# Kernel optimization log

Hardware: AMD Instinct MI355X
Metric: run time of the kernel (lower is better)

The kernel has to match this reference:

```python
import jax, jax.numpy as jnp
import numpy as np

EPS = 1e-08
ROUTING_ITERS = 3

def squash(s, axis=-1):
    norm = jnp.linalg.norm(s, axis=axis, keepdims=True)
    return norm / (1.0 + norm ** 2 + EPS) * s

def setup_inputs() -> dict:
    key = jax.random.key(0)
    k1, k2, k3 = jax.random.split(key, 3)
    B, R, C, O, I = 512, 640, 10, 16, 8
    x = jax.random.normal(k1, (B, R, I), dtype=jnp.float32)
    W = jax.random.normal(k2, (R, C, O, I), dtype=jnp.float32) * 0.01
    bias = jax.random.uniform(k3, (1, 1, C, O), dtype=jnp.float32) * 0.01
    return {"x": x, "W": W, "bias": bias}

def reference(x, W, bias):
    # u_hat[b,r,c,o] = sum_i W[r,c,o,i] * x[b,r,i]
    u_hat = jnp.einsum('rcoi,bri->brco', W, x)  # [B,R,C,O]
    u_hat_d = jax.lax.stop_gradient(u_hat)
    B, R, C, _ = u_hat.shape
    b_ij = jnp.zeros((B, R, C, 1), dtype=u_hat.dtype)
    v_j = None
    for itr in range(ROUTING_ITERS):
        c_ij = jax.nn.softmax(b_ij, axis=2)               # softmax over capsules
        s_j = jnp.sum(c_ij * u_hat_d, axis=1, keepdims=True) + bias  # [B,1,C,O]
        v_j = squash(s_j, axis=-1)
        if itr < ROUTING_ITERS - 1:
            a_ij = jnp.sum(u_hat * v_j, axis=-1, keepdims=True)  # agreement, non-detached
            b_ij = b_ij + a_ij
    return jnp.squeeze(v_j, axis=1)  # [B,C,O]
```

## Files before the change

kernel.cpp:

```cpp
#include <hip/hip_runtime.h>
#include <math.h>

#define BB 512
#define RR 640
#define CC 10
#define OO 16
#define CO 160
#define II 8
#define S_FLOATS (BB*CO)

#define NRG 40
#define RPB 16
#define WCH (RPB*CO)
#define LSTR 165
#define VSTR 164
#define VOFF 10304
#define SMEM_FLOATS (VOFF + 16*VSTR)

#define NRG_FB 8
#define RPB_FB (RR/NRG_FB)
#define ZCH (RR*CO)

using f16x8 = __attribute__((ext_vector_type(8))) _Float16;
using f32x4 = __attribute__((ext_vector_type(4))) float;



__device__ __forceinline__ float exp_small(float a) {
    float f = __builtin_fmaf(a, 0.16666667f, 0.5f);
    f = __builtin_fmaf(a, f, 1.0f);
    return __builtin_fmaf(a, f, 1.0f);
}

__device__ __forceinline__ float rowsum16(float v) {
    int t;
    t = __builtin_amdgcn_update_dpp(0, __float_as_int(v), 0x128, 0xF, 0xF, true);
    v += __int_as_float(t);
    t = __builtin_amdgcn_update_dpp(0, __float_as_int(v), 0x124, 0xF, 0xF, true);
    v += __int_as_float(t);
    t = __builtin_amdgcn_update_dpp(0, __float_as_int(v), 0x122, 0xF, 0xF, true);
    v += __int_as_float(t);
    t = __builtin_amdgcn_update_dpp(0, __float_as_int(v), 0x121, 0xF, 0xF, true);
    v += __int_as_float(t);
    return v;
}


__global__ __launch_bounds__(256) void prep(const float* __restrict__ W,
                                            const float* __restrict__ x,
                                            _Float16* __restrict__ wf,
                                            _Float16* __restrict__ xf) {
    const int t = blockIdx.x * 256 + threadIdx.x;
    if (t < RR * CO * II) wf[t] = (_Float16)W[t];
    if (t < 16) wf[RR * CO * II + t] = (_Float16)0.f;
    const int i = t & 7;
    const int b = (t >> 3) & 511;
    const int r = t >> 12;
    xf[t] = (_Float16)x[((size_t)b * RR + r) * II + i];
}


template <bool UNIFORM>
__global__ __launch_bounds__(256) void caps_pass_l(const _Float16* __restrict__ wf,
                                                   const _Float16* __restrict__ xf,
                                                   const float* __restrict__ vacc,
                                                   float* __restrict__ part) {
    __shared__ float smem[SMEM_FLOATS];
    const int tid  = threadIdx.x;
    const int lane = tid & 63;
    const int wv   = tid >> 6;
    const int n    = lane & 15;
    const int q    = lane >> 4;
    const bool q0  = (q == 0);
    const int b0   = blockIdx.x * 16;
    const int rg   = blockIdx.y;
    const int r0   = rg * RPB;

    {
        const int4* wg = reinterpret_cast<const int4*>(wf) + (size_t)r0 * CO;
        int4* ws4 = reinterpret_cast<int4*>(smem);
#pragma unroll
        for (int k = 0; k < WCH / 256; ++k)
            ws4[k * 256 + tid] = wg[k * 256 + tid];
        if (tid == 0) { int4 z; z.x = z.y = z.z = z.w = 0; ws4[WCH] = z; }
        if (!UNIFORM) {
            const float4* vg = reinterpret_cast<const float4*>(vacc);
            for (int k = tid; k < 640; k += 256) {
                const int bl = k / 40, ch = k - bl * 40;
                const float4 v = vg[(size_t)(b0 + bl) * 40 + ch];
                *reinterpret_cast<float4*>(smem + VOFF + bl * VSTR + ch * 4) = v;
            }
        }
    }
    __syncthreads();

    const f16x8* xq  = reinterpret_cast<const f16x8*>(xf);
    const int4*  ws4 = reinterpret_cast<const int4*>(smem);

    f32x4 sacc[CC];
#pragma unroll
    for (int c = 0; c < CC; ++c) sacc[c] = (f32x4){0.f, 0.f, 0.f, 0.f};

    if (UNIFORM) {
        const int rl = 4 * wv + q;
        const f16x8 bfr = xq[(size_t)(r0 + rl) * BB + b0 + n];
#pragma unroll
        for (int c = 0; c < CC; ++c) {
            const int4 a = ws4[rl * CO + c * 16 + n];
            sacc[c] = __builtin_amdgcn_mfma_f32_16x16x32_f16(
                __builtin_bit_cast(f16x8, a), bfr, sacc[c], 0, 0, 0);
        }
    } else {
        const int rl0 = wv * 4;
        f16x8 xb[4];
#pragma unroll
        for (int j = 0; j < 4; ++j)
            xb[j] = xq[(size_t)(r0 + rl0 + j) * BB + b0 + n];
        const float* vb = smem + VOFF + n * VSTR + 4 * q;

#pragma unroll
        for (int j = 0; j < 4; ++j) {
            const int rl = rl0 + j;
            f32x4 acc[CC];
#pragma unroll
            for (int c = 0; c < CC; ++c) {
                const int4 a = ws4[q0 ? (rl * CO + c * 16 + n) : WCH];
                acc[c] = __builtin_amdgcn_mfma_f32_16x16x32_f16(
                    __builtin_bit_cast(f16x8, a), xb[j],
                    (f32x4){0.f, 0.f, 0.f, 0.f}, 0, 0, 0);
            }
            float e[CC];
#pragma unroll
            for (int c = 0; c < CC; ++c) {
                const f32x4 vv = *reinterpret_cast<const f32x4*>(vb + c * 16);
                float t = acc[c][0] * vv[0] + acc[c][1] * vv[1]
                        + acc[c][2] * vv[2] + acc[c][3] * vv[3];
                t += __shfl_xor(t, 16);
                t += __shfl_xor(t, 32);
                e[c] = exp_small(t);
            }
            const float se = (((e[0] + e[1]) + (e[2] + e[3]))
                            + ((e[4] + e[5]) + (e[6] + e[7]))) + (e[8] + e[9]);
            const float inv = __fdividef(1.0f, se);
#pragma unroll
            for (int c = 0; c < CC; ++c) {
                const float w = e[c] * inv;
#pragma unroll
                for (int k = 0; k < 4; ++k)
                    sacc[c][k] = __builtin_fmaf(w, acc[c][k], sacc[c][k]);
            }
        }
    }

    __syncthreads();
    float* red = smem;
    const int cb = 4 * q;
    if (wv < 2) {
        float* dst = red + ((wv * 16 + n) * LSTR + cb);
#pragma unroll
        for (int c = 0; c < CC; ++c)
#pragma unroll
            for (int k = 0; k < 4; ++k) dst[c * 16 + k] = sacc[c][k];
    }
    __syncthreads();
    if (wv >= 2) {
        float* dst = red + (((wv - 2) * 16 + n) * LSTR + cb);
#pragma unroll
        for (int c = 0; c < CC; ++c)
#pragma unroll
            for (int k = 0; k < 4; ++k) dst[c * 16 + k] += sacc[c][k];
    }
    __syncthreads();
    if (wv == 0) {
        const float f = UNIFORM ? 0.1f : 1.0f;
        float* pb = part + (size_t)rg * S_FLOATS + (size_t)(b0 + n) * CO + cb;
        const float* ra = red + (n * LSTR + cb);
        const float* rb = red + ((16 + n) * LSTR + cb);
#pragma unroll
        for (int c = 0; c < CC; ++c) {
            f32x4 v;
#pragma unroll
            for (int k = 0; k < 4; ++k)
                v[k] = (ra[c * 16 + k] + rb[c * 16 + k]) * f;
            *reinterpret_cast<f32x4*>(pb + c * 16) = v;
        }
    }
}

__global__ __launch_bounds__(256) void caps_squash(const float* __restrict__ part,
                                                   int nsl,
                                                   const float* __restrict__ bias,
                                                   float* __restrict__ vacc,
                                                   float* __restrict__ out,
                                                   int mode) {
    const int idx = blockIdx.x * 256 + threadIdx.x;
    const int co  = idx % CO;
    float a0 = 0.f, a1 = 0.f, a2 = 0.f, a3 = 0.f;
    int s = 0;
    for (; s + 4 <= nsl; s += 4) {
        a0 += part[(size_t)s * S_FLOATS + idx];
        a1 += part[(size_t)(s + 1) * S_FLOATS + idx];
        a2 += part[(size_t)(s + 2) * S_FLOATS + idx];
        a3 += part[(size_t)(s + 3) * S_FLOATS + idx];
    }
    for (; s < nsl; ++s) a0 += part[(size_t)s * S_FLOATS + idx];
    const float val = ((a0 + a1) + (a2 + a3)) + bias[co];
    const float sq = rowsum16(val * val);
    const float norm  = sqrtf(sq);
    const float scale = norm / (1.0f + sq + 1e-8f);
    const float v = scale * val;
    if (mode == 0)      vacc[idx] = v;
    else if (mode == 1) vacc[idx] += v;
    else                out[idx] = v;
}

template <bool UNIFORM, int RPB_>
__global__ __launch_bounds__(256, 2) void caps_pass_g(const _Float16* __restrict__ wf,
                                                      const _Float16* __restrict__ xf,
                                                      const float* __restrict__ vacc,
                                                      float* __restrict__ part) {
    __shared__ float red[2 * 16 * LSTR];
    const int tid  = threadIdx.x;
    const int lane = tid & 63;
    const int wv   = tid >> 6;
    const int n    = lane & 15;
    const int q    = lane >> 4;
    const bool q0  = (q == 0);
    const int b0   = blockIdx.x * 16;
    const int rg   = blockIdx.y;
    const int r0   = rg * RPB_;

    const f16x8* xq = reinterpret_cast<const f16x8*>(xf);
    const int4*  wq = reinterpret_cast<const int4*>(wf);

    f32x4 sacc[CC];
#pragma unroll
    for (int c = 0; c < CC; ++c) sacc[c] = (f32x4){0.f, 0.f, 0.f, 0.f};

    if (UNIFORM) {
#pragma unroll 2
        for (int rr = 4 * wv; rr + 4 <= RPB_; rr += 16) {
            const int r = r0 + rr + q;
            const f16x8 bfr = xq[(size_t)r * BB + b0 + n];
#pragma unroll
            for (int c = 0; c < CC; ++c) {
                const int4 a = wq[r * CO + c * 16 + n];
                sacc[c] = __builtin_amdgcn_mfma_f32_16x16x32_f16(
                    __builtin_bit_cast(f16x8, a), bfr, sacc[c], 0, 0, 0);
            }
        }
    } else {
        f32x4 vv[CC];
        const f32x4* vp = reinterpret_cast<const f32x4*>(vacc + (size_t)(b0 + n) * CO);
#pragma unroll
        for (int c = 0; c < CC; ++c) vv[c] = vp[c * 4 + q];
#pragma unroll 2
        for (int rr = wv; rr < RPB_; rr += 4) {
            const int r = r0 + rr;
            const f16x8 bcur = xq[(size_t)r * BB + b0 + n];
            f32x4 acc[CC];
#pragma unroll
            for (int c = 0; c < CC; ++c) {
                const int4 a = wq[q0 ? (r * CO + c * 16 + n) : ZCH];
                acc[c] = __builtin_amdgcn_mfma_f32_16x16x32_f16(
                    __builtin_bit_cast(f16x8, a), bcur,
                    (f32x4){0.f, 0.f, 0.f, 0.f}, 0, 0, 0);
            }
            float e[CC];
#pragma unroll
            for (int c = 0; c < CC; ++c) {
                float t = acc[c][0] * vv[c][0] + acc[c][1] * vv[c][1]
                        + acc[c][2] * vv[c][2] + acc[c][3] * vv[c][3];
                t += __shfl_xor(t, 16);
                t += __shfl_xor(t, 32);
                e[c] = exp_small(t);
            }
            const float se = (((e[0] + e[1]) + (e[2] + e[3]))
                            + ((e[4] + e[5]) + (e[6] + e[7]))) + (e[8] + e[9]);
            const float inv = __fdividef(1.0f, se);
#pragma unroll
            for (int c = 0; c < CC; ++c) {
                const float w = e[c] * inv;
#pragma unroll
                for (int k = 0; k < 4; ++k)
                    sacc[c][k] = __builtin_fmaf(w, acc[c][k], sacc[c][k]);
            }
        }
    }

    const int cb = 4 * q;
    if (wv < 2) {
        float* dst = red + ((wv * 16 + n) * LSTR + cb);
#pragma unroll
        for (int c = 0; c < CC; ++c)
#pragma unroll
            for (int k = 0; k < 4; ++k) dst[c * 16 + k] = sacc[c][k];
    }
    __syncthreads();
    if (wv >= 2) {
        float* dst = red + (((wv - 2) * 16 + n) * LSTR + cb);
#pragma unroll
        for (int c = 0; c < CC; ++c)
#pragma unroll
            for (int k = 0; k < 4; ++k) dst[c * 16 + k] += sacc[c][k];
    }
    __syncthreads();
    if (wv == 0) {
        const float f = UNIFORM ? 0.1f : 1.0f;
        float* pb = part + (size_t)rg * S_FLOATS + (size_t)(b0 + n) * CO + cb;
        const float* ra = red + (n * LSTR + cb);
        const float* rb = red + ((16 + n) * LSTR + cb);
#pragma unroll
        for (int c = 0; c < CC; ++c) {
            f32x4 v;
#pragma unroll
            for (int k = 0; k < 4; ++k)
                v[k] = (ra[c * 16 + k] + rb[c * 16 + k]) * f;
            *reinterpret_cast<f32x4*>(pb + c * 16) = v;
        }
    }
}


extern "C" void kernel_launch(void* const* d_in, const int* in_sizes, int n_in,
                              void* d_out, int out_size, void* d_ws, size_t ws_size,
                              hipStream_t stream) {
    const float* x    = (const float*)d_in[0];
    const float* W    = (const float*)d_in[1];
    const float* bias = (const float*)d_in[2];
    float* out  = (float*)d_out;

    const int sqg = S_FLOATS / 256;

    float*    part = (float*)d_ws;
    float*    vacc = part + (size_t)NRG * S_FLOATS;
    _Float16* wf   = (_Float16*)(vacc + S_FLOATS);
    _Float16* xf   = wf + (size_t)RR * CO * II + 16;

    const size_t NEEDED = ((size_t)NRG + 1) * S_FLOATS * 4
                        + ((size_t)RR * CO * II + 16) * 2
                        + (size_t)BB * RR * II * 2;

    if (ws_size >= NEEDED) {
        prep<<<BB * RR * II / 256, 256, 0, stream>>>(W, x, wf, xf);
        const dim3 pg(32, NRG);
        caps_pass_l<true ><<<pg, 256, 0, stream>>>(wf, xf, nullptr, part);
        caps_squash<<<sqg, 256, 0, stream>>>(part, NRG, bias, vacc, out, 0);
        caps_pass_l<false><<<pg, 256, 0, stream>>>(wf, xf, vacc, part);
        caps_squash<<<sqg, 256, 0, stream>>>(part, NRG, bias, vacc, out, 1);
        caps_pass_l<false><<<pg, 256, 0, stream>>>(wf, xf, vacc, part);
        caps_squash<<<sqg, 256, 0, stream>>>(part, NRG, bias, vacc, out, 2);
    } else {
        float*    partf = (float*)d_ws;
        float*    vaccf = partf + (size_t)NRG_FB * S_FLOATS;
        _Float16* wff   = (_Float16*)(vaccf + S_FLOATS);
        _Float16* xff   = wff + (size_t)RR * CO * II + 16;
        prep<<<BB * RR * II / 256, 256, 0, stream>>>(W, x, wff, xff);
        const dim3 pg(32, NRG_FB);
        caps_pass_g<true,  RPB_FB><<<pg, 256, 0, stream>>>(wff, xff, nullptr, partf);
        caps_squash<<<sqg, 256, 0, stream>>>(partf, NRG_FB, bias, vaccf, out, 0);
        caps_pass_g<false, RPB_FB><<<pg, 256, 0, stream>>>(wff, xff, vaccf, partf);
        caps_squash<<<sqg, 256, 0, stream>>>(partf, NRG_FB, bias, vaccf, out, 1);
        caps_pass_g<false, RPB_FB><<<pg, 256, 0, stream>>>(wff, xff, vaccf, partf);
        caps_squash<<<sqg, 256, 0, stream>>>(partf, NRG_FB, bias, vaccf, out, 2);
    }
}
```

Before: 138.2 us.

## Materialize fp16 u_hat once and reuse it in later routing passes

Replaces the separate prep kernel with a first pass that converts W and x to fp16 inside the block. That pass computes u_hat with MFMA, writes the whole u_hat tensor to workspace in fp16 and produces the uniform-routing partial sums. The later routing passes read the stored u_hat instead of recomputing it with MFMA from W and x. This removes one launch and the repeated matrix products. In exchange it writes about 100 MB of u_hat once and reads it twice, which adds a lot of memory traffic and needs a much larger workspace. The fallback path is still taken if the workspace is too small.

```diff
diff --git a/kernel.cpp b/kernel.cpp
--- a/kernel.cpp
+++ b/kernel.cpp
@@ -12,10 +12,10 @@
 #define NRG 40
 #define RPB 16
 #define WCH (RPB*CO)
+#define XSTR 17
+#define XOFF (WCH*4 + 4)
 #define LSTR 165
-#define VSTR 164
-#define VOFF 10304
-#define SMEM_FLOATS (VOFF + 16*VSTR)
+#define SMEM_FLOATS (XOFF + 16*XSTR*4)
 
 #define NRG_FB 8
 #define RPB_FB (RR/NRG_FB)
@@ -45,26 +45,46 @@
     return v;
 }
 
-
-__global__ __launch_bounds__(256) void prep(const float* __restrict__ W,
-                                            const float* __restrict__ x,
-                                            _Float16* __restrict__ wf,
-                                            _Float16* __restrict__ xf) {
-    const int t = blockIdx.x * 256 + threadIdx.x;
-    if (t < RR * CO * II) wf[t] = (_Float16)W[t];
-    if (t < 16) wf[RR * CO * II + t] = (_Float16)0.f;
-    const int i = t & 7;
-    const int b = (t >> 3) & 511;
-    const int r = t >> 12;
-    xf[t] = (_Float16)x[((size_t)b * RR + r) * II + i];
-}
-
-
-template <bool UNIFORM>
-__global__ __launch_bounds__(256) void caps_pass_l(const _Float16* __restrict__ wf,
-                                                   const _Float16* __restrict__ xf,
-                                                   const float* __restrict__ vacc,
-                                                   float* __restrict__ part) {
+__device__ __forceinline__ void block_reduce_store(f32x4* sacc, float* red,
+                                                   float* part, int rg, int b0,
+                                                   int wv, int n, int q, float f) {
+    const int cb = 4 * q;
+    if (wv < 2) {
+        float* dst = red + ((wv * 16 + n) * LSTR + cb);
+#pragma unroll
+        for (int c = 0; c < CC; ++c)
+#pragma unroll
+            for (int k = 0; k < 4; ++k) dst[c * 16 + k] = sacc[c][k];
+    }
+    __syncthreads();
+    if (wv >= 2) {
+        float* dst = red + (((wv - 2) * 16 + n) * LSTR + cb);
+#pragma unroll
+        for (int c = 0; c < CC; ++c)
+#pragma unroll
+            for (int k = 0; k < 4; ++k) dst[c * 16 + k] += sacc[c][k];
+    }
+    __syncthreads();
+    if (wv == 0) {
+        float* pb = part + (size_t)rg * S_FLOATS + (size_t)(b0 + n) * CO + cb;
+        const float* ra = red + (n * LSTR + cb);
+        const float* rb = red + ((16 + n) * LSTR + cb);
+#pragma unroll
+        for (int c = 0; c < CC; ++c) {
+            f32x4 v;
+#pragma unroll
+            for (int k = 0; k < 4; ++k)
+                v[k] = (ra[c * 16 + k] + rb[c * 16 + k]) * f;
+            *reinterpret_cast<f32x4*>(pb + c * 16) = v;
+        }
+    }
+}
+
+
+__global__ __launch_bounds__(256) void caps_ugen(const float* __restrict__ W,
+                                                 const float* __restrict__ x,
+                                                 _Float16* __restrict__ u,
+                                                 float* __restrict__ part) {
     __shared__ float smem[SMEM_FLOATS];
     const int tid  = threadIdx.x;
     const int lane = tid & 63;
@@ -72,119 +92,150 @@
     const int n    = lane & 15;
     const int q    = lane >> 4;
     const bool q0  = (q == 0);
-    const int b0   = blockIdx.x * 16;
+    const int bt   = blockIdx.x;
     const int rg   = blockIdx.y;
+    const int b0   = bt * 16;
     const int r0   = rg * RPB;
 
     {
-        const int4* wg = reinterpret_cast<const int4*>(wf) + (size_t)r0 * CO;
+        const float4* wsrc = reinterpret_cast<const float4*>(W + (size_t)r0 * CO * II);
         int4* ws4 = reinterpret_cast<int4*>(smem);
 #pragma unroll
-        for (int k = 0; k < WCH / 256; ++k)
-            ws4[k * 256 + tid] = wg[k * 256 + tid];
+        for (int k = 0; k < WCH / 256; ++k) {
+            const int ch = k * 256 + tid;
+            const float4 lo = wsrc[2 * ch], hi = wsrc[2 * ch + 1];
+            f16x8 h;
+            h[0] = (_Float16)lo.x; h[1] = (_Float16)lo.y;
+            h[2] = (_Float16)lo.z; h[3] = (_Float16)lo.w;
+            h[4] = (_Float16)hi.x; h[5] = (_Float16)hi.y;
+            h[6] = (_Float16)hi.z; h[7] = (_Float16)hi.w;
+            ws4[ch] = __builtin_bit_cast(int4, h);
+        }
         if (tid == 0) { int4 z; z.x = z.y = z.z = z.w = 0; ws4[WCH] = z; }
-        if (!UNIFORM) {
-            const float4* vg = reinterpret_cast<const float4*>(vacc);
-            for (int k = tid; k < 640; k += 256) {
-                const int bl = k / 40, ch = k - bl * 40;
-                const float4 v = vg[(size_t)(b0 + bl) * 40 + ch];
-                *reinterpret_cast<float4*>(smem + VOFF + bl * VSTR + ch * 4) = v;
-            }
-        }
+        const int bl = tid >> 4, rl = tid & 15;
+        const float4* xsrc = reinterpret_cast<const float4*>(
+            x + ((size_t)(b0 + bl) * RR + r0 + rl) * II);
+        const float4 lo = xsrc[0], hi = xsrc[1];
+        f16x8 h;
+        h[0] = (_Float16)lo.x; h[1] = (_Float16)lo.y;
+        h[2] = (_Float16)lo.z; h[3] = (_Float16)lo.w;
+        h[4] = (_Float16)hi.x; h[5] = (_Float16)hi.y;
+        h[6] = (_Float16)hi.z; h[7] = (_Float16)hi.w;
+        reinterpret_cast<int4*>(smem + XOFF)[bl * XSTR + rl] =
+            __builtin_bit_cast(int4, h);
     }
     __syncthreads();
 
-    const f16x8* xq  = reinterpret_cast<const f16x8*>(xf);
-    const int4*  ws4 = reinterpret_cast<const int4*>(smem);
+    const int4* ws4 = reinterpret_cast<const int4*>(smem);
+    const int4* xs4 = reinterpret_cast<const int4*>(smem + XOFF);
+    int4* uq = reinterpret_cast<int4*>(u);
 
     f32x4 sacc[CC];
 #pragma unroll
     for (int c = 0; c < CC; ++c) sacc[c] = (f32x4){0.f, 0.f, 0.f, 0.f};
 
-    if (UNIFORM) {
-        const int rl = 4 * wv + q;
-        const f16x8 bfr = xq[(size_t)(r0 + rl) * BB + b0 + n];
+#pragma unroll
+    for (int j = 0; j < 4; ++j) {
+        const int rl = wv * 4 + j;
+        const int r  = r0 + rl;
+        const f16x8 bfr = __builtin_bit_cast(f16x8, xs4[n * XSTR + rl]);
+
+        f32x4 acc[CC];
 #pragma unroll
         for (int c = 0; c < CC; ++c) {
-            const int4 a = ws4[rl * CO + c * 16 + n];
-            sacc[c] = __builtin_amdgcn_mfma_f32_16x16x32_f16(
-                __builtin_bit_cast(f16x8, a), bfr, sacc[c], 0, 0, 0);
-        }
-    } else {
-        const int rl0 = wv * 4;
-        f16x8 xb[4];
-#pragma unroll
-        for (int j = 0; j < 4; ++j)
-            xb[j] = xq[(size_t)(r0 + rl0 + j) * BB + b0 + n];
-        const float* vb = smem + VOFF + n * VSTR + 4 * q;
-
-#pragma unroll
-        for (int j = 0; j < 4; ++j) {
-            const int rl = rl0 + j;
-            f32x4 acc[CC];
-#pragma unroll
-            for (int c = 0; c < CC; ++c) {
-                const int4 a = ws4[q0 ? (rl * CO + c * 16 + n) : WCH];
-                acc[c] = __builtin_amdgcn_mfma_f32_16x16x32_f16(
-                    __builtin_bit_cast(f16x8, a), xb[j],
-                    (f32x4){0.f, 0.f, 0.f, 0.f}, 0, 0, 0);
-            }
-            float e[CC];
-#pragma unroll
-            for (int c = 0; c < CC; ++c) {
-                const f32x4 vv = *reinterpret_cast<const f32x4*>(vb + c * 16);
-                float t = acc[c][0] * vv[0] + acc[c][1] * vv[1]
-                        + acc[c][2] * vv[2] + acc[c][3] * vv[3];
-                t += __shfl_xor(t, 16);
-                t += __shfl_xor(t, 32);
-                e[c] = exp_small(t);
-            }
-            const float se = (((e[0] + e[1]) + (e[2] + e[3]))
-                            + ((e[4] + e[5]) + (e[6] + e[7]))) + (e[8] + e[9]);
-            const float inv = __fdividef(1.0f, se);
-#pragma unroll
-            for (int c = 0; c < CC; ++c) {
-                const float w = e[c] * inv;
-#pragma unroll
-                for (int k = 0; k < 4; ++k)
-                    sacc[c][k] = __builtin_fmaf(w, acc[c][k], sacc[c][k]);
-            }
-        }
+            const int4 a = ws4[q0 ? (rl * CO + c * 16 + n) : WCH];
+            acc[c] = __builtin_amdgcn_mfma_f32_16x16x32_f16(
+                __builtin_bit_cast(f16x8, a), bfr,
+                (f32x4){0.f, 0.f, 0.f, 0.f}, 0, 0, 0);
+        }
+#pragma unroll
+        for (int p = 0; p < 5; ++p) {
+            f16x8 uo;
+#pragma unroll
+            for (int k = 0; k < 4; ++k) {
+                uo[k]     = (_Float16)acc[2 * p][k];
+                uo[4 + k] = (_Float16)acc[2 * p + 1][k];
+            }
+            uq[(((size_t)r * 32 + bt) * 5 + p) * 64 + lane] =
+                __builtin_bit_cast(int4, uo);
+        }
+#pragma unroll
+        for (int c = 0; c < CC; ++c)
+#pragma unroll
+            for (int k = 0; k < 4; ++k) sacc[c][k] += acc[c][k];
     }
 
     __syncthreads();
-    float* red = smem;
-    const int cb = 4 * q;
-    if (wv < 2) {
-        float* dst = red + ((wv * 16 + n) * LSTR + cb);
-#pragma unroll
-        for (int c = 0; c < CC; ++c)
-#pragma unroll
-            for (int k = 0; k < 4; ++k) dst[c * 16 + k] = sacc[c][k];
-    }
-    __syncthreads();
-    if (wv >= 2) {
-        float* dst = red + (((wv - 2) * 16 + n) * LSTR + cb);
-#pragma unroll
-        for (int c = 0; c < CC; ++c)
-#pragma unroll
-            for (int k = 0; k < 4; ++k) dst[c * 16 + k] += sacc[c][k];
-    }
-    __syncthreads();
-    if (wv == 0) {
-        const float f = UNIFORM ? 0.1f : 1.0f;
-        float* pb = part + (size_t)rg * S_FLOATS + (size_t)(b0 + n) * CO + cb;
-        const float* ra = red + (n * LSTR + cb);
-        const float* rb = red + ((16 + n) * LSTR + cb);
+    block_reduce_store(sacc, smem, part, rg, b0, wv, n, q, 0.1f);
+}
+
+__global__ __launch_bounds__(256) void caps_ruv(const _Float16* __restrict__ u,
+                                                const float* __restrict__ vacc,
+                                                float* __restrict__ part) {
+    __shared__ float red[2 * 16 * LSTR];
+    const int tid  = threadIdx.x;
+    const int lane = tid & 63;
+    const int wv   = tid >> 6;
+    const int n    = lane & 15;
+    const int q    = lane >> 4;
+    const int bt   = blockIdx.x;
+    const int rg   = blockIdx.y;
+    const int b0   = bt * 16;
+    const int r0   = rg * RPB;
+
+    const int4* uq = reinterpret_cast<const int4*>(u);
+
+    f32x4 vv[CC];
+    const f32x4* vp = reinterpret_cast<const f32x4*>(vacc + (size_t)(b0 + n) * CO);
+#pragma unroll
+    for (int c = 0; c < CC; ++c) vv[c] = vp[c * 4 + q];
+
+    f32x4 sacc[CC];
+#pragma unroll
+    for (int c = 0; c < CC; ++c) sacc[c] = (f32x4){0.f, 0.f, 0.f, 0.f};
+
+#pragma unroll 2
+    for (int j = 0; j < 4; ++j) {
+        const int r = r0 + wv * 4 + j;
+
+        int4 uc[5];
+#pragma unroll
+        for (int p = 0; p < 5; ++p)
+            uc[p] = uq[(((size_t)r * 32 + bt) * 5 + p) * 64 + lane];
+
+        f32x4 acc[CC];
+#pragma unroll
+        for (int p = 0; p < 5; ++p) {
+            const f16x8 h = __builtin_bit_cast(f16x8, uc[p]);
+#pragma unroll
+            for (int k = 0; k < 4; ++k) {
+                acc[2 * p][k]     = (float)h[k];
+                acc[2 * p + 1][k] = (float)h[4 + k];
+            }
+        }
+
+        float e[CC];
 #pragma unroll
         for (int c = 0; c < CC; ++c) {
-            f32x4 v;
+            float t = acc[c][0] * vv[c][0] + acc[c][1] * vv[c][1]
+                    + acc[c][2] * vv[c][2] + acc[c][3] * vv[c][3];
+            t += __shfl_xor(t, 16);
+            t += __shfl_xor(t, 32);
+            e[c] = exp_small(t);
+        }
+        const float se = (((e[0] + e[1]) + (e[2] + e[3]))
+                        + ((e[4] + e[5]) + (e[6] + e[7]))) + (e[8] + e[9]);
+        const float inv = __fdividef(1.0f, se);
+#pragma unroll
+        for (int c = 0; c < CC; ++c) {
+            const float w = e[c] * inv;
 #pragma unroll
             for (int k = 0; k < 4; ++k)
-                v[k] = (ra[c * 16 + k] + rb[c * 16 + k]) * f;
-            *reinterpret_cast<f32x4*>(pb + c * 16) = v;
-        }
-    }
+                sacc[c][k] = __builtin_fmaf(w, acc[c][k], sacc[c][k]);
+        }
+    }
+
+    block_reduce_store(sacc, red, part, rg, b0, wv, n, q, 1.0f);
 }
 
 __global__ __launch_bounds__(256) void caps_squash(const float* __restrict__ part,
@@ -214,6 +265,19 @@
     else                out[idx] = v;
 }
 
+__global__ __launch_bounds__(256) void prep(const float* __restrict__ W,
+                                            const float* __restrict__ x,
+                                            _Float16* __restrict__ wf,
+                                            _Float16* __restrict__ xf) {
+    const int t = blockIdx.x * 256 + threadIdx.x;
+    if (t < RR * CO * II) wf[t] = (_Float16)W[t];
+    if (t < 16) wf[RR * CO * II + t] = (_Float16)0.f;
+    const int i = t & 7;
+    const int b = (t >> 3) & 511;
+    const int r = t >> 12;
+    xf[t] = (_Float16)x[((size_t)b * RR + r) * II + i];
+}
+
 template <bool UNIFORM, int RPB_>
 __global__ __launch_bounds__(256, 2) void caps_pass_g(const _Float16* __restrict__ wf,
                                                       const _Float16* __restrict__ xf,
@@ -287,38 +351,7 @@
             }
         }
     }
-
-    const int cb = 4 * q;
-    if (wv < 2) {
-        float* dst = red + ((wv * 16 + n) * LSTR + cb);
-#pragma unroll
-        for (int c = 0; c < CC; ++c)
-#pragma unroll
-            for (int k = 0; k < 4; ++k) dst[c * 16 + k] = sacc[c][k];
-    }
-    __syncthreads();
-    if (wv >= 2) {
-        float* dst = red + (((wv - 2) * 16 + n) * LSTR + cb);
-#pragma unroll
-        for (int c = 0; c < CC; ++c)
-#pragma unroll
-            for (int k = 0; k < 4; ++k) dst[c * 16 + k] += sacc[c][k];
-    }
-    __syncthreads();
-    if (wv == 0) {
-        const float f = UNIFORM ? 0.1f : 1.0f;
-        float* pb = part + (size_t)rg * S_FLOATS + (size_t)(b0 + n) * CO + cb;
-        const float* ra = red + (n * LSTR + cb);
-        const float* rb = red + ((16 + n) * LSTR + cb);
-#pragma unroll
-        for (int c = 0; c < CC; ++c) {
-            f32x4 v;
-#pragma unroll
-            for (int k = 0; k < 4; ++k)
-                v[k] = (ra[c * 16 + k] + rb[c * 16 + k]) * f;
-            *reinterpret_cast<f32x4*>(pb + c * 16) = v;
-        }
-    }
+    block_reduce_store(sacc, red, part, rg, b0, wv, n, q, UNIFORM ? 0.1f : 1.0f);
 }
 
 
@@ -334,21 +367,18 @@
 
     float*    part = (float*)d_ws;
     float*    vacc = part + (size_t)NRG * S_FLOATS;
-    _Float16* wf   = (_Float16*)(vacc + S_FLOATS);
-    _Float16* xf   = wf + (size_t)RR * CO * II + 16;
+    _Float16* uu   = (_Float16*)(vacc + S_FLOATS);
 
     const size_t NEEDED = ((size_t)NRG + 1) * S_FLOATS * 4
-                        + ((size_t)RR * CO * II + 16) * 2
-                        + (size_t)BB * RR * II * 2;
+                        + (size_t)RR * BB * CO * 2;
 
     if (ws_size >= NEEDED) {
-        prep<<<BB * RR * II / 256, 256, 0, stream>>>(W, x, wf, xf);
         const dim3 pg(32, NRG);
-        caps_pass_l<true ><<<pg, 256, 0, stream>>>(wf, xf, nullptr, part);
+        caps_ugen<<<pg, 256, 0, stream>>>(W, x, uu, part);
         caps_squash<<<sqg, 256, 0, stream>>>(part, NRG, bias, vacc, out, 0);
-        caps_pass_l<false><<<pg, 256, 0, stream>>>(wf, xf, vacc, part);
+        caps_ruv<<<pg, 256, 0, stream>>>(uu, vacc, part);
         caps_squash<<<sqg, 256, 0, stream>>>(part, NRG, bias, vacc, out, 1);
-        caps_pass_l<false><<<pg, 256, 0, stream>>>(wf, xf, vacc, part);
+        caps_ruv<<<pg, 256, 0, stream>>>(uu, vacc, part);
         caps_squash<<<sqg, 256, 0, stream>>>(part, NRG, bias, vacc, out, 2);
     } else {
         float*    partf = (float*)d_ws;
```

New measurement: 149.0 us. +7.8%, slower.
